# Kernel optimization log

Hardware: AMD Instinct MI355X
Metric: run time of the kernel (lower is better)

## Reference

```python
import jax, jax.numpy as jnp
import numpy as np

NUM_ORI = 16
DEGREE = 2
NUM_LAYERS = 2
LN_EPS = 1e-6


def ori_grid_s1(n):
    theta = jnp.linspace(0.0, 2.0 * jnp.pi, n + 1)[:-1]
    return jnp.stack([jnp.cos(theta), jnp.sin(theta)], axis=-1)  # (O, 2)


def poly_feats(z, degree):
    # PolynomialFeatures: [z, z*z outer, (z*z)*z outer ...] flattened
    feats = [z]
    p = z
    for _ in range(degree):
        p = (p[..., :, None] * z[..., None, :]).reshape(*z.shape[:-1], -1)
        feats.append(p)
    return jnp.concatenate(feats, axis=-1)


def basis_mlp(z, W1, b1, W2, b2):
    return jax.nn.gelu(jax.nn.gelu(z @ W1 + b1) @ W2 + b2)


def layer_norm(h, scale, bias):
    mu = h.mean(axis=-1, keepdims=True)
    var = ((h - mu) ** 2).mean(axis=-1, keepdims=True)
    return (h - mu) * jax.lax.rsqrt(var + LN_EPS) * scale + bias


def setup_inputs() -> dict:
    key = jax.random.key(0)
    ks = jax.random.split(key, 16)
    B, N, NIN, H, BD, WF, OUT, L = 1, 256, 3, 64, 32, 4, 3, NUM_LAYERS
    s = 0.05
    return {
        'pos': jax.random.normal(ks[0], (B, N, 2), jnp.float32),
        'x': jax.random.normal(ks[1], (B, N, NIN), jnp.float32),
        'skb_W1': jax.random.normal(ks[2], (14, H), jnp.float32) * s,
        'skb_b1': jnp.zeros((H,), jnp.float32),
        'skb_W2': jax.random.normal(ks[3], (H, BD), jnp.float32) * s,
        'skb_b2': jnp.zeros((BD,), jnp.float32),
        'rkb_W1': jax.random.normal(ks[4], (3, H), jnp.float32) * s,
        'rkb_b1': jnp.zeros((H,), jnp.float32),
        'rkb_W2': jax.random.normal(ks[5], (H, BD), jnp.float32) * s,
        'rkb_b2': jnp.zeros((BD,), jnp.float32),
        'emb_W': jax.random.normal(ks[6], (NIN, H), jnp.float32) * s,
        'conv_sW': jax.random.normal(ks[7], (L, BD, H), jnp.float32) * s,
        'conv_rW': jax.random.normal(ks[8], (L, BD, H), jnp.float32) * s,
        'conv_b': jnp.zeros((L, H), jnp.float32),
        'ln_scale': jnp.ones((L, H), jnp.float32),
        'ln_bias': jnp.zeros((L, H), jnp.float32),
        'lin1_W': jax.random.normal(ks[9], (L, H, WF * H), jnp.float32) * s,
        'lin1_b': jnp.zeros((L, WF * H), jnp.float32),
        'lin2_W': jax.random.normal(ks[10], (L, WF * H, H), jnp.float32) * s,
        'lin2_b': jnp.zeros((L, H), jnp.float32),
        'readout_W': jax.random.normal(ks[11], (H, OUT), jnp.float32) * s,
    }


def reference(pos, x, skb_W1, skb_b1, skb_W2, skb_b2, rkb_W1, rkb_b1, rkb_W2, rkb_b2,
              emb_W, conv_sW, conv_rW, conv_b, ln_scale, ln_bias,
              lin1_W, lin1_b, lin2_W, lin2_b, readout_W):
    ori = ori_grid_s1(NUM_ORI)  # (O, 2)
    # rel_pos: (B, n, m, 1, 2) -> broadcast against ori (O, 2)
    rel_pos = pos[:, None, :, None, :] - pos[:, :, None, None, :]
    inv1 = jnp.sum(rel_pos * ori[None, None, None, :, :], axis=-1, keepdims=True)  # (B,N,N,O,1)
    inv2 = jnp.linalg.norm(rel_pos - rel_pos * inv1, axis=-1, keepdims=True)       # (B,N,N,O,1)
    spatial_inv = jnp.concatenate([inv1, inv2], axis=-1)                            # (B,N,N,O,2)
    orient_inv = jnp.sum(ori[:, None, :] * ori[None, :, :], axis=-1, keepdims=True) # (O,O,1)

    kernel_basis = basis_mlp(poly_feats(spatial_inv, DEGREE), skb_W1, skb_b1, skb_W2, skb_b2)  # (B,N,N,O,BD)
    fiber_basis = basis_mlp(poly_feats(orient_inv, DEGREE), rkb_W1, rkb_b1, rkb_W2, rkb_b2)    # (O,O,BD)

    h = x @ emb_W                                  # (B,N,H)
    O = NUM_ORI
    h = jnp.broadcast_to(h[:, :, None, :], (h.shape[0], h.shape[1], O, h.shape[2]))  # (B,N,O,H)

    for i in range(NUM_LAYERS):
        inp = h
        sk = kernel_basis @ conv_sW[i]             # (B,N,N,O,H)
        rk = fiber_basis @ conv_rW[i]              # (O,O,H)
        c = jnp.einsum('bnoc,bmnoc->bmoc', h, sk)  # spatial aggregation
        c = jnp.einsum('bmoc,poc->bmpc', c, rk)    # orientation mixing
        c = c + conv_b[i]
        c = layer_norm(c, ln_scale[i], ln_bias[i])
        c = jax.nn.gelu(c @ lin1_W[i] + lin1_b[i]) @ lin2_W[i] + lin2_b[i]
        h = inp + c

    readout = h @ readout_W                        # (B,N,O,OUT)
    out_scalar = readout.mean(axis=-2)             # (B,N,OUT)
    out_scalar = jnp.sum(out_scalar, axis=1) / out_scalar.shape[1]  # global pool -> (B,OUT)
    return out_scalar
```

## Files before the change

### kernel.cpp

```cpp
#include <hip/hip_runtime.h>
#include <math.h>

#define NPTS 256
#define NORI 16
#define CH   64
#define BD   32
#define HID  64
#define STEP16 0.39269908169872414f

typedef __bf16 bf16x8 __attribute__((ext_vector_type(8)));
typedef float  f32x4  __attribute__((ext_vector_type(4)));

#define MFMA16(a, b, cc) __builtin_amdgcn_mfma_f32_16x16x32_bf16(a, b, cc, 0, 0, 0)
#define GLOAD_LDS16NT(g, l) \
    __builtin_amdgcn_global_load_lds((const __attribute__((address_space(1))) unsigned int*)(g), \
                                     (__attribute__((address_space(3))) unsigned int*)(l), 16, 0, 2)

__device__ __forceinline__ float gelu_f(float x) {
    float x2 = x * x;
    float y2 = x * fmaf(0.07135481627f, x2, 1.5957691216f);
    float e = __expf(y2);
    return x - x * __builtin_amdgcn_rcpf(e + 1.0f);
}

__device__ __forceinline__ unsigned pk2(float x, float y) {
    union { __bf16 h[2]; unsigned u; } r;
    r.h[0] = (__bf16)x; r.h[1] = (__bf16)y;
    return r.u;
}

__device__ __forceinline__ void dev_prep(
    const float* __restrict__ skb_W1, const float* __restrict__ skb_W2,
    const float* __restrict__ conv_sW,
    __bf16* __restrict__ w1T, __bf16* __restrict__ w2T, __bf16* __restrict__ w2Tlo,
    __bf16* __restrict__ sWT, __bf16* __restrict__ sWTlo, int t)
{
    if (t < 64) {
        float f[9];
        f[0] = skb_W1[t];
        f[1] = skb_W1[64 + t];
        f[2] = skb_W1[128 + t];
        f[3] = skb_W1[192 + t] + skb_W1[256 + t];
        f[4] = skb_W1[320 + t];
        f[5] = skb_W1[384 + t];
        f[6] = skb_W1[448 + t] + skb_W1[512 + t] + skb_W1[640 + t];
        f[7] = skb_W1[576 + t] + skb_W1[704 + t] + skb_W1[768 + t];
        f[8] = skb_W1[832 + t];
#pragma unroll
        for (int k = 0; k < 9; ++k) {
            __bf16 hi = (__bf16)f[k];
            w1T[t * 32 + k]      = hi;
            w1T[t * 32 + 9 + k]  = (__bf16)(f[k] - (float)hi);
            w1T[t * 32 + 18 + k] = hi;
        }
#pragma unroll
        for (int k = 27; k < 32; ++k) w1T[t * 32 + k] = (__bf16)0.0f;
    }
    for (int i = t; i < 2048; i += 256) {
        int n = i >> 6, kk = i & 63;
        float v = skb_W2[kk * 32 + n];
        __bf16 hi = (__bf16)v;
        w2T[i]   = hi;
        w2Tlo[i] = (__bf16)(v - (float)hi);
    }
    for (int i = t; i < 4096; i += 256) {
        int ll = i >> 11, chh = (i >> 5) & 63, k = i & 31;
        float v = conv_sW[(ll * 32 + k) * 64 + chh];
        __bf16 hi = (__bf16)v;
        sWT[i]   = hi;
        sWTlo[i] = (__bf16)(v - (float)hi);
    }
}

__device__ __forceinline__ void dev_fiber(
    const float* __restrict__ rkb_W1, const float* __restrict__ rkb_b1,
    const float* __restrict__ rkb_W2, const float* __restrict__ rkb_b2,
    const float* __restrict__ conv_rW, float* __restrict__ rk, int p, int t)
{
    __shared__ float w1L[3 * 64], b1L[64], w2L[64 * 32], b2L[32];
    __shared__ float rwL[2 * 32 * 64];
    __shared__ float t1L[16 * 64];
    __shared__ float fbL[16 * 32];

    if (t < 192) w1L[t] = rkb_W1[t];
    if (t >= 192 && t < 256) b1L[t - 192] = rkb_b1[t - 192];
    for (int i = t; i < 2048; i += 256) w2L[i] = rkb_W2[i];
    if (t < 32) b2L[t] = rkb_b2[t];
    for (int i = t; i < 4096; i += 256) rwL[i] = conv_rW[i];
    __syncthreads();

    const int o = t & 15;
    const float cp = cosf(p * STEP16), sp = sinf(p * STEP16);
    const float co = cosf(o * STEP16), so = sinf(o * STEP16);
    const float s0 = cp * co + sp * so;
    const float m1 = s0 * s0, m2 = m1 * s0;

    {
        const int jg = t >> 4;
#pragma unroll
        for (int u = 0; u < 4; ++u) {
            const int j = jg * 4 + u;
            float a = b1L[j] + s0 * w1L[j] + m1 * w1L[64 + j] + m2 * w1L[128 + j];
            t1L[o * 64 + j] = gelu_f(a);
        }
    }
    __syncthreads();
    {
        const int kg = t >> 4;
#pragma unroll
        for (int kk = 0; kk < 2; ++kk) {
            const int k = kg + kk * 16;
            float a = b2L[k];
#pragma unroll
            for (int j = 0; j < 64; ++j) a += t1L[o * 64 + j] * w2L[j * 32 + k];
            fbL[o * 32 + k] = gelu_f(a);
        }
    }
    __syncthreads();
    {
        const int o2 = t >> 4;
        const int chg = (t & 15) * 4;
#pragma unroll
        for (int l = 0; l < 2; ++l) {
            f32x4 acc = {0.f, 0.f, 0.f, 0.f};
#pragma unroll
            for (int k = 0; k < 32; ++k) {
                const float fv = fbL[o2 * 32 + k];
                const f32x4 rv = *(const f32x4*)(rwL + (l * 32 + k) * 64 + chg);
                acc[0] = fmaf(fv, rv[0], acc[0]);
                acc[1] = fmaf(fv, rv[1], acc[1]);
                acc[2] = fmaf(fv, rv[2], acc[2]);
                acc[3] = fmaf(fv, rv[3], acc[3]);
            }
            *(f32x4*)(rk + (l * 256 + p * 16 + o2) * 64 + chg) = acc;
        }
    }
}

__global__ __launch_bounds__(256) void k_prep(
    const float* __restrict__ skb_W1, const float* __restrict__ skb_W2,
    const float* __restrict__ conv_sW,
    __bf16* __restrict__ w1T, __bf16* __restrict__ w2T, __bf16* __restrict__ w2Tlo,
    __bf16* __restrict__ sWT, __bf16* __restrict__ sWTlo)
{
    dev_prep(skb_W1, skb_W2, conv_sW, w1T, w2T, w2Tlo, sWT, sWTlo, threadIdx.x);
}

__global__ __launch_bounds__(256) void k_fiber2(
    const float* __restrict__ rkb_W1, const float* __restrict__ rkb_b1,
    const float* __restrict__ rkb_W2, const float* __restrict__ rkb_b2,
    const float* __restrict__ conv_rW, float* __restrict__ rk)
{
    dev_fiber(rkb_W1, rkb_b1, rkb_W2, rkb_b2, conv_rW, rk, blockIdx.x, threadIdx.x);
}

__global__ __launch_bounds__(256) void k_init(
    const float* __restrict__ x, const float* __restrict__ emb_W, float* __restrict__ h)
{
    int idx = blockIdx.x * 256 + threadIdx.x;
    int ch = idx & 63;
    int n  = idx >> 10;
    h[idx] = x[n * 3] * emb_W[ch] + x[n * 3 + 1] * emb_W[64 + ch] + x[n * 3 + 2] * emb_W[128 + ch];
}

__global__ __launch_bounds__(256) void k_setup(
    const float* __restrict__ x, const float* __restrict__ emb_W, float* __restrict__ h2,
    const float* __restrict__ rkb_W1, const float* __restrict__ rkb_b1,
    const float* __restrict__ rkb_W2, const float* __restrict__ rkb_b2,
    const float* __restrict__ conv_rW, float* __restrict__ rk,
    const float* __restrict__ skb_W1, const float* __restrict__ skb_W2,
    const float* __restrict__ conv_sW,
    __bf16* __restrict__ w1T, __bf16* __restrict__ w2T, __bf16* __restrict__ w2Tlo,
    __bf16* __restrict__ sWT, __bf16* __restrict__ sWTlo)
{
    const int b = blockIdx.x, t = threadIdx.x;
    if (b < 1024) {
        int idx = b * 256 + t;
        int ch = (idx >> 4) & 63;
        int n  = idx >> 10;
        h2[idx] = x[n * 3] * emb_W[ch] + x[n * 3 + 1] * emb_W[64 + ch]
                + x[n * 3 + 2] * emb_W[128 + ch];
    } else if (b < 1040) {
        dev_fiber(rkb_W1, rkb_b1, rkb_W2, rkb_b2, conv_rW, rk, b - 1024, t);
    } else {
        dev_prep(skb_W1, skb_W2, conv_sW, w1T, w2T, w2Tlo, sWT, sWTlo, t);
    }
}

__global__ __launch_bounds__(256) void k_kb2(
    const float* __restrict__ pos,
    const float* __restrict__ skb_b1, const float* __restrict__ skb_b2,
    const __bf16* __restrict__ w1T, const __bf16* __restrict__ w2T,
    const __bf16* __restrict__ w2Tlo, __bf16* __restrict__ kb_g)
{
    const int t = threadIdx.x;
    const int c = t & 15, qq = (t >> 4) & 3, w = t >> 6;
    const int b = blockIdx.x;
    const int pair = b >> 2;
    const int ohalf = (b >> 1) & 1;
    const int mhalf = b & 1;
    const int m0 = (pair >> 4) * 16, n0 = (pair & 15) * 16;

    bf16x8 w1B[4], w2A[2][2], w2Alo[2][2];
    float b1x[4][4], b2x[2][4];
#pragma unroll
    for (int ni = 0; ni < 4; ++ni) {
        w1B[ni] = *(const bf16x8*)(w1T + (ni * 16 + c) * 32 + qq * 8);
#pragma unroll
        for (int r = 0; r < 4; ++r) b1x[ni][r] = skb_b1[ni * 16 + qq * 4 + r];
    }
#pragma unroll
    for (int mk = 0; mk < 2; ++mk) {
#pragma unroll
        for (int ks = 0; ks < 2; ++ks) {
            w2A[mk][ks]   = *(const bf16x8*)(w2T   + (mk * 16 + c) * 64 + ks * 32 + qq * 8);
            w2Alo[mk][ks] = *(const bf16x8*)(w2Tlo + (mk * 16 + c) * 64 + ks * 32 + qq * 8);
        }
#pragma unroll
        for (int r = 0; r < 4; ++r) b2x[mk][r] = skb_b2[mk * 16 + qq * 4 + r];
    }

    const int n = n0 + c;
    const float pnx = pos[2 * n], pny = pos[2 * n + 1];
    float cosv[4], sinv[4];
#pragma unroll
    for (int oi = 0; oi < 4; ++oi) {
        float th = (float)(ohalf * 4 + oi) * STEP16;
        cosv[oi] = cosf(th); sinv[oi] = sinf(th);
    }
    const int s0lane = c + ((qq & 1) << 5);
    const int s1lane = s0lane + 16;
    const int selhi = qq >> 1;
    const f32x4 zf = {0.f, 0.f, 0.f, 0.f};

#pragma unroll 1
    for (int mi2 = 0; mi2 < 2; ++mi2) {
        const int m = m0 + w * 4 + mhalf * 2 + mi2;
        const float dx = pnx - pos[2 * m];
        const float dy = pny - pos[2 * m + 1];
#pragma unroll
        for (int oi = 0; oi < 4; ++oi) {
            const int o = ohalf * 4 + oi;
            float a = dx * cosv[oi] + dy * sinv[oi];
            float vx = dx - dx * a, vy = dy - dy * a;
            float b2 = sqrtf(vx * vx + vy * vy);
            float mfv[9];
            mfv[0] = a; mfv[1] = b2; mfv[2] = a * a; mfv[3] = a * b2; mfv[4] = b2 * b2;
            mfv[5] = mfv[2] * a; mfv[6] = mfv[2] * b2; mfv[7] = mfv[3] * b2; mfv[8] = mfv[4] * b2;
            __bf16 mh[9], ml[9];
#pragma unroll
            for (int i = 0; i < 9; ++i) {
                mh[i] = (__bf16)mfv[i];
                ml[i] = (__bf16)(mfv[i] - (float)mh[i]);
            }
            bf16x8 mb;
            if (qq == 0) {
                mb[0]=mh[0]; mb[1]=mh[1]; mb[2]=mh[2]; mb[3]=mh[3];
                mb[4]=mh[4]; mb[5]=mh[5]; mb[6]=mh[6]; mb[7]=mh[7];
            } else if (qq == 1) {
                mb[0]=mh[8]; mb[1]=mh[0]; mb[2]=mh[1]; mb[3]=mh[2];
                mb[4]=mh[3]; mb[5]=mh[4]; mb[6]=mh[5]; mb[7]=mh[6];
            } else if (qq == 2) {
                mb[0]=mh[7]; mb[1]=mh[8]; mb[2]=ml[0]; mb[3]=ml[1];
                mb[4]=ml[2]; mb[5]=ml[3]; mb[6]=ml[4]; mb[7]=ml[5];
            } else {
                mb[0]=ml[6]; mb[1]=ml[7]; mb[2]=ml[8]; mb[3]=(__bf16)0.0f;
                mb[4]=(__bf16)0.0f; mb[5]=(__bf16)0.0f; mb[6]=(__bf16)0.0f; mb[7]=(__bf16)0.0f;
            }

            unsigned t1p[4][2];
#pragma unroll
            for (int ni = 0; ni < 4; ++ni) {
                f32x4 acc = MFMA16(w1B[ni], mb, zf);
                float g0 = gelu_f(acc[0] + b1x[ni][0]);
                float g1 = gelu_f(acc[1] + b1x[ni][1]);
                float g2 = gelu_f(acc[2] + b1x[ni][2]);
                float g3 = gelu_f(acc[3] + b1x[ni][3]);
                t1p[ni][0] = pk2(g0, g1);
                t1p[ni][1] = pk2(g2, g3);
            }

            bf16x8 B2[2];
#pragma unroll
            for (int ks = 0; ks < 2; ++ks) {
                const unsigned lo0 = t1p[ks * 2][0],     lo1 = t1p[ks * 2][1];
                const unsigned hi0 = t1p[ks * 2 + 1][0], hi1 = t1p[ks * 2 + 1][1];
                unsigned aL0 = (unsigned)__shfl((int)lo0, s0lane);
                unsigned aL1 = (unsigned)__shfl((int)lo1, s0lane);
                unsigned aL2 = (unsigned)__shfl((int)lo0, s1lane);
                unsigned aL3 = (unsigned)__shfl((int)lo1, s1lane);
                unsigned aH0 = (unsigned)__shfl((int)hi0, s0lane);
                unsigned aH1 = (unsigned)__shfl((int)hi1, s0lane);
                unsigned aH2 = (unsigned)__shfl((int)hi0, s1lane);
                unsigned aH3 = (unsigned)__shfl((int)hi1, s1lane);
                union { unsigned u[4]; bf16x8 v; } bu;
                bu.u[0] = selhi ? aH0 : aL0;
                bu.u[1] = selhi ? aH1 : aL1;
                bu.u[2] = selhi ? aH2 : aL2;
                bu.u[3] = selhi ? aH3 : aL3;
                B2[ks] = bu.v;
            }

            const size_t ptP = (size_t)((m * 256 + n) * 16 + o);
            const size_t ptM = (size_t)((n * 256 + m) * 16 + (o ^ 8));
            const int swz = o & 3;
#pragma unroll
            for (int mk = 0; mk < 2; ++mk) {
                f32x4 acc = MFMA16(w2A[mk][0], B2[0], zf);
                acc = MFMA16(w2A[mk][1], B2[1], acc);
                acc = MFMA16(w2Alo[mk][0], B2[0], acc);
                acc = MFMA16(w2Alo[mk][1], B2[1], acc);
                float g0 = gelu_f(acc[0] + b2x[mk][0]);
                float g1 = gelu_f(acc[1] + b2x[mk][1]);
                float g2 = gelu_f(acc[2] + b2x[mk][2]);
                float g3 = gelu_f(acc[3] + b2x[mk][3]);
                uint2 pv; pv.x = pk2(g0, g1); pv.y = pk2(g2, g3);
                const int off = (((mk * 2 + (qq >> 1)) ^ swz) << 4) + ((qq & 1) << 3);
                *(uint2*)((char*)kb_g + ptP * 64 + off) = pv;
                *(uint2*)((char*)kb_g + ptM * 64 + off) = pv;
            }
        }
    }
}

__global__ __launch_bounds__(1024) void k_conv4(
    const __bf16* __restrict__ kb_g,
    const __bf16* __restrict__ sWT, const __bf16* __restrict__ sWTlo,
    const float* __restrict__ conv_b, const float* __restrict__ rkg,
    const float* __restrict__ ln_scale, const float* __restrict__ ln_bias,
    const float* __restrict__ lin1_W, const float* __restrict__ lin1_b,
    const float* __restrict__ lin2_W, const float* __restrict__ lin2_b,
    const float* __restrict__ h_in, float* __restrict__ h_out, int l)
{
    __shared__ __align__(16) unsigned char smem[90112];
    const int t = threadIdx.x;
    const int m = blockIdx.x;
    const int w = t >> 6, lane = t & 63;
    const int qq = lane >> 4, c = lane & 15;
    const f32x4 zf = {0.f, 0.f, 0.f, 0.f};

    bf16x8 sWB[4], sWBlo[4];
#pragma unroll
    for (int ni = 0; ni < 4; ++ni) {
        sWB[ni]   = *(const bf16x8*)(sWT   + l * 2048 + (ni * 16 + c) * 32 + qq * 8);
        sWBlo[ni] = *(const bf16x8*)(sWTlo + l * 2048 + (ni * 16 + c) * 32 + qq * 8);
    }

    f32x4 cacc[4];
#pragma unroll
    for (int ni = 0; ni < 4; ++ni)
#pragma unroll
        for (int r = 0; r < 4; ++r) cacc[ni][r] = 0.f;

    const char* kbm = (const char*)kb_g + (size_t)m * 262144;
    const char* gsrc0 = kbm + w * 1024 + lane * 16;
    char* lbase = (char*)smem + w * 1024;
    const int myrow = (w * 16 + c) * 64 + ((qq ^ (c & 3)) << 4);

    GLOAD_LDS16NT(gsrc0, lbase);
    f32x4 hc0, hc1, hc2, hc3;
    {
        const float* hp = h_in + w * 1024 + c * 16 + qq * 4;
        hc0 = *(const f32x4*)(hp);
        hc1 = *(const f32x4*)(hp + 256);
        hc2 = *(const f32x4*)(hp + 512);
        hc3 = *(const f32x4*)(hp + 768);
    }

#pragma unroll 1
    for (int tile = 0; tile < 15; ++tile) {
        const int bufoff = (tile & 1) << 14;
        GLOAD_LDS16NT(gsrc0 + (size_t)(tile + 1) * 16384, lbase + (bufoff ^ 16384));
        asm volatile("s_waitcnt vmcnt(5)" ::: "memory");
        __builtin_amdgcn_sched_barrier(0);
        bf16x8 aF = *(const bf16x8*)(smem + bufoff + myrow);

        const float* hpn = h_in + ((tile + 1) * 16 + w) * 1024 + c * 16 + qq * 4;
        f32x4 hn0 = *(const f32x4*)(hpn);
        f32x4 hn1 = *(const f32x4*)(hpn + 256);
        f32x4 hn2 = *(const f32x4*)(hpn + 512);
        f32x4 hn3 = *(const f32x4*)(hpn + 768);

        f32x4 g;
        g = MFMA16(aF, sWB[0], zf);
        g = MFMA16(aF, sWBlo[0], g);
#pragma unroll
        for (int r = 0; r < 4; ++r) cacc[0][r] = fmaf(g[r], hc0[r], cacc[0][r]);
        g = MFMA16(aF, sWB[1], zf);
        g = MFMA16(aF, sWBlo[1], g);
#pragma unroll
        for (int r = 0; r < 4; ++r) cacc[1][r] = fmaf(g[r], hc1[r], cacc[1][r]);
        g = MFMA16(aF, sWB[2], zf);
        g = MFMA16(aF, sWBlo[2], g);
#pragma unroll
        for (int r = 0; r < 4; ++r) cacc[2][r] = fmaf(g[r], hc2[r], cacc[2][r]);
        g = MFMA16(aF, sWB[3], zf);
        g = MFMA16(aF, sWBlo[3], g);
#pragma unroll
        for (int r = 0; r < 4; ++r) cacc[3][r] = fmaf(g[r], hc3[r], cacc[3][r]);

        hc0 = hn0; hc1 = hn1; hc2 = hn2; hc3 = hn3;
    }
    {
        asm volatile("s_waitcnt vmcnt(4)" ::: "memory");
        __builtin_amdgcn_sched_barrier(0);
        bf16x8 aF = *(const bf16x8*)(smem + ((15 & 1) << 14) + myrow);
        f32x4 g;
        g = MFMA16(aF, sWB[0], zf);
        g = MFMA16(aF, sWBlo[0], g);
#pragma unroll
        for (int r = 0; r < 4; ++r) cacc[0][r] = fmaf(g[r], hc0[r], cacc[0][r]);
        g = MFMA16(aF, sWB[1], zf);
        g = MFMA16(aF, sWBlo[1], g);
#pragma unroll
        for (int r = 0; r < 4; ++r) cacc[1][r] = fmaf(g[r], hc1[r], cacc[1][r]);
        g = MFMA16(aF, sWB[2], zf);
        g = MFMA16(aF, sWBlo[2], g);
#pragma unroll
        for (int r = 0; r < 4; ++r) cacc[2][r] = fmaf(g[r], hc2[r], cacc[2][r]);
        g = MFMA16(aF, sWB[3], zf);
        g = MFMA16(aF, sWBlo[3], g);
#pragma unroll
        for (int r = 0; r < 4; ++r) cacc[3][r] = fmaf(g[r], hc3[r], cacc[3][r]);
    }
    __syncthreads();

    {
        float* c1p = (float*)smem;
#pragma unroll
        for (int ni = 0; ni < 4; ++ni)
#pragma unroll
            for (int r = 0; r < 4; ++r)
                c1p[w * 1024 + (qq * 4 + r) * 64 + ni * 16 + c] = cacc[ni][r];
    }
    __syncthreads();
    {
        float* c1p = (float*)smem;
        float* c1r = (float*)(smem + 65536);
        float s = 0.f;
#pragma unroll
        for (int ww = 0; ww < 16; ++ww) s += c1p[ww * 1024 + t];
        c1r[t] = s;
    }
    __syncthreads();

    {
        float* c1r = (float*)(smem + 65536);
        float* cns = (float*)(smem + 69632);
        const int ch = lane;
        const float cb  = conv_b[l * 64 + ch];
        const float lsc = ln_scale[l * 64 + ch], lbi = ln_bias[l * 64 + ch];
        const float* rkp = rkg + (l * 256 + w * 16) * 64 + ch;
        float s = cb;
#pragma unroll
        for (int o = 0; o < 16; ++o) s += c1r[o * 64 + ch] * rkp[o * 64];
        float red = s;
#pragma unroll
        for (int off = 32; off > 0; off >>= 1) red += __shfl_xor(red, off);
        float mu = red * (1.0f / 64.0f);
        float d = s - mu;
        float r2 = d * d;
#pragma unroll
        for (int off = 32; off > 0; off >>= 1) r2 += __shfl_xor(r2, off);
        cns[w * 64 + ch] = d * rsqrtf(r2 * (1.0f / 64.0f) + 1e-6f) * lsc + lbi;
    }
    __syncthreads();

    {
        float* cns = (float*)(smem + 69632);
        float* usS = (float*)(smem + 73728);
        const int j = t & 255, q4 = t >> 8;
        const float* W1l = lin1_W + l * 64 * 256;
        const float bl1 = lin1_b[l * 256 + j];
        float ua[4];
#pragma unroll
        for (int pi = 0; pi < 4; ++pi) ua[pi] = bl1;
#pragma unroll 4
        for (int c2 = 0; c2 < 64; ++c2) {
            const float wv = W1l[c2 * 256 + j];
#pragma unroll
            for (int pi = 0; pi < 4; ++pi)
                ua[pi] = fmaf(cns[(q4 * 4 + pi) * 64 + c2], wv, ua[pi]);
        }
#pragma unroll
        for (int pi = 0; pi < 4; ++pi) usS[(q4 * 4 + pi) * 256 + j] = gelu_f(ua[pi]);
    }
    __syncthreads();

    {
        float* usS = (float*)(smem + 73728);
        const int ch2 = t & 63, pg = t >> 6;
        const float* W2l = lin2_W + l * 256 * 64;
        float o0 = lin2_b[l * 64 + ch2];
#pragma unroll 4
        for (int j = 0; j < 256; ++j)
            o0 = fmaf(usS[pg * 256 + j], W2l[j * 64 + ch2], o0);
        const int i0 = m * 1024 + ch2 * 16 + pg;
        h_out[i0] = h_in[i0] + o0;
    }
}

__global__ __launch_bounds__(512, 1) void k_layer2(
    const float* __restrict__ pos,
    const float* __restrict__ skb_b1, const float* __restrict__ skb_b2,
    const __bf16* __restrict__ w1T, const __bf16* __restrict__ w2T,
    const __bf16* __restrict__ w2Tlo,
    const __bf16* __restrict__ sWT, const __bf16* __restrict__ sWTlo,
    const float* __restrict__ conv_b, const float* __restrict__ rkg,
    const float* __restrict__ ln_scale, const float* __restrict__ ln_bias,
    const float* __restrict__ lin1_W, const float* __restrict__ lin1_b,
    const float* __restrict__ lin2_W, const float* __restrict__ lin2_b,
    const float* __restrict__ h_in, float* __restrict__ h_out, int l)
{
    __shared__ __align__(16) unsigned char smem[57344];
    const int t = threadIdx.x;
    const int m = blockIdx.x;
    const int w = t >> 6, lane = t & 63;
    const int qq = lane >> 4, c = lane & 15;

    bf16x8 w1B[4], sWB[4], sWBlo[4], w2B[2][2], w2Blo[2][2];
    float b1v[4], b2v[2];
#pragma unroll
    for (int ni = 0; ni < 4; ++ni) {
        w1B[ni]   = *(const bf16x8*)(w1T + (ni * 16 + c) * 32 + qq * 8);
        sWB[ni]   = *(const bf16x8*)(sWT   + l * 2048 + (ni * 16 + c) * 32 + qq * 8);
        sWBlo[ni] = *(const bf16x8*)(sWTlo + l * 2048 + (ni * 16 + c) * 32 + qq * 8);
        b1v[ni] = skb_b1[ni * 16 + c];
    }
#pragma unroll
    for (int nt = 0; nt < 2; ++nt) {
        b2v[nt] = skb_b2[nt * 16 + c];
#pragma unroll
        for (int ks = 0; ks < 2; ++ks) {
            w2B[nt][ks]   = *(const bf16x8*)(w2T   + (nt * 16 + c) * 64 + ks * 32 + qq * 8);
            w2Blo[nt][ks] = *(const bf16x8*)(w2Tlo + (nt * 16 + c) * 64 + ks * 32 + qq * 8);
        }
    }

    const float pmx = pos[2 * m], pmy = pos[2 * m + 1];
    float co_ = 0.f, so_ = 0.f;
    if (t < 256) { float th = (float)(t & 15) * STEP16; co_ = cosf(th); so_ = sinf(th); }

    f32x4 cacc[4];
#pragma unroll
    for (int ni = 0; ni < 4; ++ni)
#pragma unroll
        for (int r = 0; r < 4; ++r) cacc[ni][r] = 0.f;

#pragma unroll 1
    for (int tile = 0; tile < 16; ++tile) {
        if (t < 256) {
            const int n = tile * 16 + (t >> 4);
            float dx = pos[2 * n] - pmx, dy = pos[2 * n + 1] - pmy;
            float a = dx * co_ + dy * so_;
            float vx = dx - dx * a, vy = dy - dy * a;
            float b = sqrtf(vx * vx + vy * vy);
            float mf[9];
            mf[0] = a; mf[1] = b; mf[2] = a * a; mf[3] = a * b; mf[4] = b * b;
            mf[5] = mf[2] * a; mf[6] = mf[2] * b; mf[7] = mf[3] * b; mf[8] = mf[4] * b;
            __bf16 s[32];
#pragma unroll
            for (int i = 0; i < 9; ++i) {
                __bf16 hi = (__bf16)mf[i];
                s[i] = hi; s[9 + i] = hi;
                s[18 + i] = (__bf16)(mf[i] - (float)hi);
            }
#pragma unroll
            for (int i = 27; i < 32; ++i) s[i] = (__bf16)0.0f;
            unsigned char* rowp = smem + t * 64;
#pragma unroll
            for (int u = 0; u < 4; ++u) {
                bf16x8 vv;
#pragma unroll
                for (int j = 0; j < 8; ++j) vv[j] = s[u * 8 + j];
                *(bf16x8*)(rowp + ((u ^ (t & 3)) << 4)) = vv;
            }
        }
        __syncthreads();

#pragma unroll
        for (int mm = 0; mm < 2; ++mm) {
            const int row = (2 * w + mm) * 16 + c;
            bf16x8 aF = *(const bf16x8*)(smem + row * 64 + ((qq ^ (row & 3)) << 4));
#pragma unroll
            for (int ni = 0; ni < 4; ++ni) {
                f32x4 acc = {0.f, 0.f, 0.f, 0.f};
                acc = MFMA16(aF, w1B[ni], acc);
#pragma unroll
                for (int r = 0; r < 4; ++r) {
                    const int ro = (2 * w + mm) * 16 + qq * 4 + r;
                    float g = gelu_f(acc[r] + b1v[ni]);
                    const int chc = ni * 16 + c;
                    *(__bf16*)(smem + 16384 + ro * 128 + (((chc >> 3) ^ (ro & 7)) << 4)
                               + ((chc & 7) << 1)) = (__bf16)g;
                }
            }
        }
        __syncthreads();

#pragma unroll
        for (int mm = 0; mm < 2; ++mm) {
            const int row = (2 * w + mm) * 16 + c;
            bf16x8 a0 = *(const bf16x8*)(smem + 16384 + row * 128 + ((qq ^ (row & 7)) << 4));
            bf16x8 a1 = *(const bf16x8*)(smem + 16384 + row * 128 + (((4 + qq) ^ (row & 7)) << 4));
#pragma unroll
            for (int nt = 0; nt < 2; ++nt) {
                f32x4 acc = {0.f, 0.f, 0.f, 0.f};
                acc = MFMA16(a0, w2B[nt][0], acc);
                acc = MFMA16(a1, w2B[nt][1], acc);
                acc = MFMA16(a0, w2Blo[nt][0], acc);
                acc = MFMA16(a1, w2Blo[nt][1], acc);
#pragma unroll
                for (int r = 0; r < 4; ++r) {
                    const int ro = (2 * w + mm) * 16 + qq * 4 + r;
                    float g = gelu_f(acc[r] + b2v[nt]);
                    const int kc = nt * 16 + c;
                    *(__bf16*)(smem + ro * 64 + (((kc >> 3) ^ (ro & 3)) << 4)
                               + ((kc & 7) << 1)) = (__bf16)g;
                }
            }
        }
        __syncthreads();

#pragma unroll
        for (int mm = 0; mm < 2; ++mm) {
            const int mi = 2 * w + mm;
            const int row = mi * 16 + c;
            bf16x8 aF = *(const bf16x8*)(smem + row * 64 + ((qq ^ (row & 3)) << 4));
            const int nbase = (tile * 16 + mi) * 1024 + qq * 256;
#pragma unroll
            for (int ni = 0; ni < 4; ++ni) {
                f32x4 g3 = {0.f, 0.f, 0.f, 0.f};
                g3 = MFMA16(aF, sWB[ni], g3);
                g3 = MFMA16(aF, sWBlo[ni], g3);
#pragma unroll
                for (int r = 0; r < 4; ++r) {
                    float hv = h_in[nbase + r * 64 + ni * 16 + c];
                    cacc[ni][r] = fmaf(g3[r], hv, cacc[ni][r]);
                }
            }
        }
        __syncthreads();
    }

    {
        float* c1p = (float*)smem;
#pragma unroll
        for (int ni = 0; ni < 4; ++ni)
#pragma unroll
            for (int r = 0; r < 4; ++r)
                c1p[w * 1024 + (qq * 4 + r) * 64 + ni * 16 + c] = cacc[ni][r];
    }
    __syncthreads();
    {
        float* c1p = (float*)smem;
        float* c1r = (float*)(smem + 32768);
        for (int i = t; i < 1024; i += 512) {
            float s = 0.f;
#pragma unroll
            for (int ww = 0; ww < 8; ++ww) s += c1p[ww * 1024 + i];
            c1r[i] = s;
        }
    }
    __syncthreads();

    {
        float* c1r = (float*)(smem + 32768);
        float* cns = (float*)(smem + 36864);
        const int ch = lane;
        const float cb  = conv_b[l * 64 + ch];
        const float lsc = ln_scale[l * 64 + ch], lbi = ln_bias[l * 64 + ch];
#pragma unroll
        for (int pp = 0; pp < 2; ++pp) {
            const int p = w + pp * 8;
            const float* rkp = rkg + (l * 256 + p * 16) * 64 + ch;
            float s = cb;
#pragma unroll
            for (int o = 0; o < 16; ++o) s += c1r[o * 64 + ch] * rkp[o * 64];
            float red = s;
#pragma unroll
            for (int off = 32; off > 0; off >>= 1) red += __shfl_xor(red, off);
            float mu = red * (1.0f / 64.0f);
            float d = s - mu;
            float r2 = d * d;
#pragma unroll
            for (int off = 32; off > 0; off >>= 1) r2 += __shfl_xor(r2, off);
            cns[p * 64 + ch] = d * rsqrtf(r2 * (1.0f / 64.0f) + 1e-6f) * lsc + lbi;
        }
    }
    __syncthreads();

    {
        float* cns = (float*)(smem + 36864);
        float* usS = (float*)(smem + 40960);
        const int j = t & 255, half = t >> 8;
        const float* W1l = lin1_W + l * 64 * 256;
        const float bl1 = lin1_b[l * 256 + j];
        float ua[8];
#pragma unroll
        for (int pi = 0; pi < 8; ++pi) ua[pi] = bl1;
#pragma unroll 1
        for (int c2 = 0; c2 < 64; ++c2) {
            const float wv = W1l[c2 * 256 + j];
#pragma unroll
            for (int pi = 0; pi < 8; ++pi)
                ua[pi] = fmaf(cns[(half * 8 + pi) * 64 + c2], wv, ua[pi]);
        }
#pragma unroll
        for (int pi = 0; pi < 8; ++pi) usS[(half * 8 + pi) * 256 + j] = gelu_f(ua[pi]);
    }
    __syncthreads();

    {
        float* usS = (float*)(smem + 40960);
        const int ch2 = t & 63, pg = t >> 6;
        const float* W2l = lin2_W + l * 256 * 64;
        const float bl2 = lin2_b[l * 64 + ch2];
        float o0 = bl2, o1 = bl2;
#pragma unroll 2
        for (int j = 0; j < 256; ++j) {
            const float wv = W2l[j * 64 + ch2];
            o0 = fmaf(usS[pg * 256 + j], wv, o0);
            o1 = fmaf(usS[(pg + 8) * 256 + j], wv, o1);
        }
        const int i0 = (m * 16 + pg) * 64 + ch2;
        const int i1 = (m * 16 + pg + 8) * 64 + ch2;
        h_out[i0] = h_in[i0] + o0;
        h_out[i1] = h_in[i1] + o1;
    }
}

__global__ __launch_bounds__(256) void k_readout_part(
    const float* __restrict__ h, float* __restrict__ part16)
{
    __shared__ float part[4][64];
    const int t = threadIdx.x, b = blockIdx.x;
    const int c = t & 63, seg = t >> 6;
    float s = 0.f;
    const int r0 = b * 256 + seg * 64;
    for (int r = r0; r < r0 + 64; ++r) s += h[r * 64 + c];
    part[seg][c] = s;
    __syncthreads();
    if (t < 64) part16[b * 64 + t] = part[0][t] + part[1][t] + part[2][t] + part[3][t];
}

__global__ __launch_bounds__(256) void k_readout_part2(
    const float* __restrict__ h, float* __restrict__ part16)
{
    const int t = threadIdx.x, b = blockIdx.x;
    const int ch = t >> 2, oq = t & 3;
    float s = 0.f;
#pragma unroll
    for (int nn = 0; nn < 16; ++nn) {
        const int n = b * 16 + nn;
        f32x4 v = *(const f32x4*)(h + n * 1024 + ch * 16 + oq * 4);
        s += (v[0] + v[1]) + (v[2] + v[3]);
    }
    s += __shfl_xor(s, 1);
    s += __shfl_xor(s, 2);
    if (oq == 0) part16[b * 64 + ch] = s;
}

__global__ __launch_bounds__(64) void k_readout_final(
    const float* __restrict__ part16, const float* __restrict__ rW, float* __restrict__ out)
{
    __shared__ float hbar[64];
    const int t = threadIdx.x;
    float s = 0.f;
#pragma unroll
    for (int b = 0; b < 16; ++b) s += part16[b * 64 + t];
    hbar[t] = s * (1.0f / 4096.0f);
    __syncthreads();
    if (t < 3) {
        float s2 = 0.f;
#pragma unroll
        for (int k = 0; k < 64; ++k) s2 += hbar[k] * rW[k * 3 + t];
        out[t] = s2;
    }
}

extern "C" void kernel_launch(void* const* d_in, const int* in_sizes, int n_in,
                              void* d_out, int out_size, void* d_ws, size_t ws_size,
                              hipStream_t stream)
{
    const float* pos      = (const float*)d_in[0];
    const float* x        = (const float*)d_in[1];
    const float* skb_W1   = (const float*)d_in[2];
    const float* skb_b1   = (const float*)d_in[3];
    const float* skb_W2   = (const float*)d_in[4];
    const float* skb_b2   = (const float*)d_in[5];
    const float* rkb_W1   = (const float*)d_in[6];
    const float* rkb_b1   = (const float*)d_in[7];
    const float* rkb_W2   = (const float*)d_in[8];
    const float* rkb_b2   = (const float*)d_in[9];
    const float* emb_W    = (const float*)d_in[10];
    const float* conv_sW  = (const float*)d_in[11];
    const float* conv_rW  = (const float*)d_in[12];
    const float* conv_b   = (const float*)d_in[13];
    const float* ln_scale = (const float*)d_in[14];
    const float* ln_bias  = (const float*)d_in[15];
    const float* lin1_W   = (const float*)d_in[16];
    const float* lin1_b   = (const float*)d_in[17];
    const float* lin2_W   = (const float*)d_in[18];
    const float* lin2_b   = (const float*)d_in[19];
    const float* readout_W= (const float*)d_in[20];
    float* out = (float*)d_out;

    unsigned char* ws = (unsigned char*)d_ws;
    float*  h_a    = (float*)(ws);
    float*  h_b    = (float*)(ws + 1048576);
    float*  rkw    = (float*)(ws + 2097152);
    __bf16* w1T    = (__bf16*)(ws + 2228224);
    __bf16* w2T    = (__bf16*)(ws + 2232320);
    __bf16* w2Tlo  = (__bf16*)(ws + 2236416);
    __bf16* sWT    = (__bf16*)(ws + 2240512);
    __bf16* sWTlo  = (__bf16*)(ws + 2248704);
    float*  part16 = (float*)(ws + 2256896);
    __bf16* kb_g   = (__bf16*)(ws + 2260992);

    const bool fast = (ws_size >= 2260992ull + 67108864ull);

    if (fast) {
        k_setup<<<1041, 256, 0, stream>>>(x, emb_W, h_a,
                                          rkb_W1, rkb_b1, rkb_W2, rkb_b2, conv_rW, rkw,
                                          skb_W1, skb_W2, conv_sW,
                                          w1T, w2T, w2Tlo, sWT, sWTlo);
        k_kb2<<<1024, 256, 0, stream>>>(pos, skb_b1, skb_b2, w1T, w2T, w2Tlo, kb_g);
        k_conv4<<<256, 1024, 0, stream>>>(kb_g, sWT, sWTlo, conv_b, rkw,
                                          ln_scale, ln_bias, lin1_W, lin1_b,
                                          lin2_W, lin2_b, h_a, h_b, 0);
        k_conv4<<<256, 1024, 0, stream>>>(kb_g, sWT, sWTlo, conv_b, rkw,
                                          ln_scale, ln_bias, lin1_W, lin1_b,
                                          lin2_W, lin2_b, h_b, h_a, 1);
        k_readout_part2<<<16, 256, 0, stream>>>(h_a, part16);
        k_readout_final<<<1, 64, 0, stream>>>(part16, readout_W, out);
    } else {
        k_prep<<<1, 256, 0, stream>>>(skb_W1, skb_W2, conv_sW, w1T, w2T, w2Tlo, sWT, sWTlo);
        k_fiber2<<<16, 256, 0, stream>>>(rkb_W1, rkb_b1, rkb_W2, rkb_b2, conv_rW, rkw);
        k_init<<<1024, 256, 0, stream>>>(x, emb_W, h_a);
        k_layer2<<<256, 512, 0, stream>>>(pos, skb_b1, skb_b2, w1T, w2T, w2Tlo, sWT, sWTlo,
                                          conv_b, rkw, ln_scale, ln_bias, lin1_W, lin1_b,
                                          lin2_W, lin2_b, h_a, h_b, 0);
        k_layer2<<<256, 512, 0, stream>>>(pos, skb_b1, skb_b2, w1T, w2T, w2Tlo, sWT, sWTlo,
                                          conv_b, rkw, ln_scale, ln_bias, lin1_W, lin1_b,
                                          lin2_W, lin2_b, h_b, h_a, 1);
        k_readout_part<<<16, 256, 0, stream>>>(h_a, part16);
        k_readout_final<<<1, 64, 0, stream>>>(part16, readout_W, out);
    }
}
```

Before: 146.2 us.

## Split conv kernel into half-N aggregation blocks plus separate epilogue kernel

The fused per-point conv kernel is split in two. The spatial aggregation now runs over 512 blocks, each covering half of the neighbour range and writing partial sums to a global workspace. A separate epilogue kernel adds the two halves and does orientation mixing, layer norm and the MLP. The aim is more parallelism and occupancy (launch bounds allow 2 blocks per CU, with smaller LDS) and overlap of the memory-bound kb streaming. The cost is two extra kernel launches per forward pass and a global round-trip of the partial sums.

Result: slower. 162.5 us (+11.2%).

```diff
diff --git a/kernel.cpp b/kernel.cpp
--- a/kernel.cpp
+++ b/kernel.cpp
@@ -323,180 +323,199 @@
     }
 }
 
-__global__ __launch_bounds__(1024) void k_conv4(
+__global__ __launch_bounds__(1024, 2) void k_convm(
     const __bf16* __restrict__ kb_g,
     const __bf16* __restrict__ sWT, const __bf16* __restrict__ sWTlo,
+    const float* __restrict__ h_in, float* __restrict__ c1part, int l)
+{
+    __shared__ __align__(16) unsigned char smem[65536];
+    const int t = threadIdx.x;
+    const int m = blockIdx.x >> 1, half = blockIdx.x & 1;
+    const int w = t >> 6, lane = t & 63;
+    const int qq = lane >> 4, c = lane & 15;
+    const f32x4 zf = {0.f, 0.f, 0.f, 0.f};
+
+    bf16x8 sWB[4], sWBlo[4];
+#pragma unroll
+    for (int ni = 0; ni < 4; ++ni) {
+        sWB[ni]   = *(const bf16x8*)(sWT   + l * 2048 + (ni * 16 + c) * 32 + qq * 8);
+        sWBlo[ni] = *(const bf16x8*)(sWTlo + l * 2048 + (ni * 16 + c) * 32 + qq * 8);
+    }
+
+    f32x4 cacc[4];
+#pragma unroll
+    for (int ni = 0; ni < 4; ++ni)
+#pragma unroll
+        for (int r = 0; r < 4; ++r) cacc[ni][r] = 0.f;
+
+    const char* kbm = (const char*)kb_g + (size_t)m * 262144 + (size_t)half * 131072;
+    const char* gsrc0 = kbm + w * 1024 + lane * 16;
+    char* lbase = (char*)smem + w * 1024;
+    const int myrow = (w * 16 + c) * 64 + ((qq ^ (c & 3)) << 4);
+    const int n00 = half * 128 + w;
+
+    GLOAD_LDS16NT(gsrc0, lbase);
+    f32x4 hc0, hc1, hc2, hc3;
+    {
+        const float* hp = h_in + n00 * 1024 + c * 16 + qq * 4;
+        hc0 = *(const f32x4*)(hp);
+        hc1 = *(const f32x4*)(hp + 256);
+        hc2 = *(const f32x4*)(hp + 512);
+        hc3 = *(const f32x4*)(hp + 768);
+    }
+
+#pragma unroll 1
+    for (int tt = 0; tt < 7; ++tt) {
+        const int bufoff = (tt & 1) << 14;
+        GLOAD_LDS16NT(gsrc0 + (size_t)(tt + 1) * 16384, lbase + (bufoff ^ 16384));
+        asm volatile("s_waitcnt vmcnt(5)" ::: "memory");
+        __builtin_amdgcn_sched_barrier(0);
+        bf16x8 aF = *(const bf16x8*)(smem + bufoff + myrow);
+
+        const float* hpn = h_in + (n00 + (tt + 1) * 16) * 1024 + c * 16 + qq * 4;
+        f32x4 hn0 = *(const f32x4*)(hpn);
+        f32x4 hn1 = *(const f32x4*)(hpn + 256);
+        f32x4 hn2 = *(const f32x4*)(hpn + 512);
+        f32x4 hn3 = *(const f32x4*)(hpn + 768);
+
+        f32x4 g;
+        g = MFMA16(aF, sWB[0], zf);
+        g = MFMA16(aF, sWBlo[0], g);
+#pragma unroll
+        for (int r = 0; r < 4; ++r) cacc[0][r] = fmaf(g[r], hc0[r], cacc[0][r]);
+        g = MFMA16(aF, sWB[1], zf);
+        g = MFMA16(aF, sWBlo[1], g);
+#pragma unroll
+        for (int r = 0; r < 4; ++r) cacc[1][r] = fmaf(g[r], hc1[r], cacc[1][r]);
+        g = MFMA16(aF, sWB[2], zf);
+        g = MFMA16(aF, sWBlo[2], g);
+#pragma unroll
+        for (int r = 0; r < 4; ++r) cacc[2][r] = fmaf(g[r], hc2[r], cacc[2][r]);
+        g = MFMA16(aF, sWB[3], zf);
+        g = MFMA16(aF, sWBlo[3], g);
+#pragma unroll
+        for (int r = 0; r < 4; ++r) cacc[3][r] = fmaf(g[r], hc3[r], cacc[3][r]);
+
+        hc0 = hn0; hc1 = hn1; hc2 = hn2; hc3 = hn3;
+    }
+    {
+        asm volatile("s_waitcnt vmcnt(4)" ::: "memory");
+        __builtin_amdgcn_sched_barrier(0);
+        bf16x8 aF = *(const bf16x8*)(smem + ((7 & 1) << 14) + myrow);
+        f32x4 g;
+        g = MFMA16(aF, sWB[0], zf);
+        g = MFMA16(aF, sWBlo[0], g);
+#pragma unroll
+        for (int r = 0; r < 4; ++r) cacc[0][r] = fmaf(g[r], hc0[r], cacc[0][r]);
+        g = MFMA16(aF, sWB[1], zf);
+        g = MFMA16(aF, sWBlo[1], g);
+#pragma unroll
+        for (int r = 0; r < 4; ++r) cacc[1][r] = fmaf(g[r], hc1[r], cacc[1][r]);
+        g = MFMA16(aF, sWB[2], zf);
+        g = MFMA16(aF, sWBlo[2], g);
+#pragma unroll
+        for (int r = 0; r < 4; ++r) cacc[2][r] = fmaf(g[r], hc2[r], cacc[2][r]);
+        g = MFMA16(aF, sWB[3], zf);
+        g = MFMA16(aF, sWBlo[3], g);
+#pragma unroll
+        for (int r = 0; r < 4; ++r) cacc[3][r] = fmaf(g[r], hc3[r], cacc[3][r]);
+    }
+    __syncthreads();
+
+    {
+        float* c1p = (float*)smem;
+#pragma unroll
+        for (int ni = 0; ni < 4; ++ni)
+#pragma unroll
+            for (int r = 0; r < 4; ++r)
+                c1p[w * 1024 + (qq * 4 + r) * 64 + ni * 16 + c] = cacc[ni][r];
+    }
+    __syncthreads();
+    {
+        float* c1p = (float*)smem;
+        float s = 0.f;
+#pragma unroll
+        for (int ww = 0; ww < 16; ++ww) s += c1p[ww * 1024 + t];
+        c1part[(half * 256 + m) * 1024 + t] = s;
+    }
+}
+
+__global__ __launch_bounds__(512) void k_convepi(
+    const float* __restrict__ c1part,
     const float* __restrict__ conv_b, const float* __restrict__ rkg,
     const float* __restrict__ ln_scale, const float* __restrict__ ln_bias,
     const float* __restrict__ lin1_W, const float* __restrict__ lin1_b,
     const float* __restrict__ lin2_W, const float* __restrict__ lin2_b,
     const float* __restrict__ h_in, float* __restrict__ h_out, int l)
 {
-    __shared__ __align__(16) unsigned char smem[90112];
+    __shared__ float c1r[1024];
+    __shared__ float cns[1024];
+    __shared__ float usS[4096];
     const int t = threadIdx.x;
     const int m = blockIdx.x;
     const int w = t >> 6, lane = t & 63;
-    const int qq = lane >> 4, c = lane & 15;
-    const f32x4 zf = {0.f, 0.f, 0.f, 0.f};
-
-    bf16x8 sWB[4], sWBlo[4];
-#pragma unroll
-    for (int ni = 0; ni < 4; ++ni) {
-        sWB[ni]   = *(const bf16x8*)(sWT   + l * 2048 + (ni * 16 + c) * 32 + qq * 8);
-        sWBlo[ni] = *(const bf16x8*)(sWTlo + l * 2048 + (ni * 16 + c) * 32 + qq * 8);
-    }
-
-    f32x4 cacc[4];
-#pragma unroll
-    for (int ni = 0; ni < 4; ++ni)
-#pragma unroll
-        for (int r = 0; r < 4; ++r) cacc[ni][r] = 0.f;
-
-    const char* kbm = (const char*)kb_g + (size_t)m * 262144;
-    const char* gsrc0 = kbm + w * 1024 + lane * 16;
-    char* lbase = (char*)smem + w * 1024;
-    const int myrow = (w * 16 + c) * 64 + ((qq ^ (c & 3)) << 4);
-
-    GLOAD_LDS16NT(gsrc0, lbase);
-    f32x4 hc0, hc1, hc2, hc3;
-    {
-        const float* hp = h_in + w * 1024 + c * 16 + qq * 4;
-        hc0 = *(const f32x4*)(hp);
-        hc1 = *(const f32x4*)(hp + 256);
-        hc2 = *(const f32x4*)(hp + 512);
-        hc3 = *(const f32x4*)(hp + 768);
-    }
-
-#pragma unroll 1
-    for (int tile = 0; tile < 15; ++tile) {
-        const int bufoff = (tile & 1) << 14;
-        GLOAD_LDS16NT(gsrc0 + (size_t)(tile + 1) * 16384, lbase + (bufoff ^ 16384));
-        asm volatile("s_waitcnt vmcnt(5)" ::: "memory");
-        __builtin_amdgcn_sched_barrier(0);
-        bf16x8 aF = *(const bf16x8*)(smem + bufoff + myrow);
-
-        const float* hpn = h_in + ((tile + 1) * 16 + w) * 1024 + c * 16 + qq * 4;
-        f32x4 hn0 = *(const f32x4*)(hpn);
-        f32x4 hn1 = *(const f32x4*)(hpn + 256);
-        f32x4 hn2 = *(const f32x4*)(hpn + 512);
-        f32x4 hn3 = *(const f32x4*)(hpn + 768);
-
-        f32x4 g;
-        g = MFMA16(aF, sWB[0], zf);
-        g = MFMA16(aF, sWBlo[0], g);
-#pragma unroll
-        for (int r = 0; r < 4; ++r) cacc[0][r] = fmaf(g[r], hc0[r], cacc[0][r]);
-        g = MFMA16(aF, sWB[1], zf);
-        g = MFMA16(aF, sWBlo[1], g);
-#pragma unroll
-        for (int r = 0; r < 4; ++r) cacc[1][r] = fmaf(g[r], hc1[r], cacc[1][r]);
-        g = MFMA16(aF, sWB[2], zf);
-        g = MFMA16(aF, sWBlo[2], g);
-#pragma unroll
-        for (int r = 0; r < 4; ++r) cacc[2][r] = fmaf(g[r], hc2[r], cacc[2][r]);
-        g = MFMA16(aF, sWB[3], zf);
-        g = MFMA16(aF, sWBlo[3], g);
-#pragma unroll
-        for (int r = 0; r < 4; ++r) cacc[3][r] = fmaf(g[r], hc3[r], cacc[3][r]);
-
-        hc0 = hn0; hc1 = hn1; hc2 = hn2; hc3 = hn3;
-    }
-    {
-        asm volatile("s_waitcnt vmcnt(4)" ::: "memory");
-        __builtin_amdgcn_sched_barrier(0);
-        bf16x8 aF = *(const bf16x8*)(smem + ((15 & 1) << 14) + myrow);
-        f32x4 g;
-        g = MFMA16(aF, sWB[0], zf);
-        g = MFMA16(aF, sWBlo[0], g);
-#pragma unroll
-        for (int r = 0; r < 4; ++r) cacc[0][r] = fmaf(g[r], hc0[r], cacc[0][r]);
-        g = MFMA16(aF, sWB[1], zf);
-        g = MFMA16(aF, sWBlo[1], g);
-#pragma unroll
-        for (int r = 0; r < 4; ++r) cacc[1][r] = fmaf(g[r], hc1[r], cacc[1][r]);
-        g = MFMA16(aF, sWB[2], zf);
-        g = MFMA16(aF, sWBlo[2], g);
-#pragma unroll
-        for (int r = 0; r < 4; ++r) cacc[2][r] = fmaf(g[r], hc2[r], cacc[2][r]);
-        g = MFMA16(aF, sWB[3], zf);
-        g = MFMA16(aF, sWBlo[3], g);
-#pragma unroll
-        for (int r = 0; r < 4; ++r) cacc[3][r] = fmaf(g[r], hc3[r], cacc[3][r]);
-    }
-    __syncthreads();
-
-    {
-        float* c1p = (float*)smem;
-#pragma unroll
-        for (int ni = 0; ni < 4; ++ni)
-#pragma unroll
-            for (int r = 0; r < 4; ++r)
-                c1p[w * 1024 + (qq * 4 + r) * 64 + ni * 16 + c] = cacc[ni][r];
-    }
-    __syncthreads();
-    {
-        float* c1p = (float*)smem;
-        float* c1r = (float*)(smem + 65536);
-        float s = 0.f;
-#pragma unroll
-        for (int ww = 0; ww < 16; ++ww) s += c1p[ww * 1024 + t];
-        c1r[t] = s;
-    }
-    __syncthreads();
-
-    {
-        float* c1r = (float*)(smem + 65536);
-        float* cns = (float*)(smem + 69632);
+
+    for (int i = t; i < 1024; i += 512)
+        c1r[i] = c1part[m * 1024 + i] + c1part[(256 + m) * 1024 + i];
+    __syncthreads();
+
+    {
         const int ch = lane;
         const float cb  = conv_b[l * 64 + ch];
         const float lsc = ln_scale[l * 64 + ch], lbi = ln_bias[l * 64 + ch];
-        const float* rkp = rkg + (l * 256 + w * 16) * 64 + ch;
-        float s = cb;
-#pragma unroll
-        for (int o = 0; o < 16; ++o) s += c1r[o * 64 + ch] * rkp[o * 64];
-        float red = s;
-#pragma unroll
-        for (int off = 32; off > 0; off >>= 1) red += __shfl_xor(red, off);
-        float mu = red * (1.0f / 64.0f);
-        float d = s - mu;
-        float r2 = d * d;
-#pragma unroll
-        for (int off = 32; off > 0; off >>= 1) r2 += __shfl_xor(r2, off);
-        cns[w * 64 + ch] = d * rsqrtf(r2 * (1.0f / 64.0f) + 1e-6f) * lsc + lbi;
-    }
-    __syncthreads();
-
-    {
-        float* cns = (float*)(smem + 69632);
-        float* usS = (float*)(smem + 73728);
-        const int j = t & 255, q4 = t >> 8;
+#pragma unroll
+        for (int pp = 0; pp < 2; ++pp) {
+            const int p = w + pp * 8;
+            const float* rkp = rkg + (l * 256 + p * 16) * 64 + ch;
+            float s = cb;
+#pragma unroll
+            for (int o = 0; o < 16; ++o) s += c1r[o * 64 + ch] * rkp[o * 64];
+            float red = s;
+#pragma unroll
+            for (int off = 32; off > 0; off >>= 1) red += __shfl_xor(red, off);
+            float mu = red * (1.0f / 64.0f);
+            float d = s - mu;
+            float r2 = d * d;
+#pragma unroll
+            for (int off = 32; off > 0; off >>= 1) r2 += __shfl_xor(r2, off);
+            cns[p * 64 + ch] = d * rsqrtf(r2 * (1.0f / 64.0f) + 1e-6f) * lsc + lbi;
+        }
+    }
+    __syncthreads();
+
+    {
+        const int j = t & 255, hf = t >> 8;
         const float* W1l = lin1_W + l * 64 * 256;
         const float bl1 = lin1_b[l * 256 + j];
-        float ua[4];
-#pragma unroll
-        for (int pi = 0; pi < 4; ++pi) ua[pi] = bl1;
+        float ua[8];
+#pragma unroll
+        for (int pi = 0; pi < 8; ++pi) ua[pi] = bl1;
 #pragma unroll 4
         for (int c2 = 0; c2 < 64; ++c2) {
             const float wv = W1l[c2 * 256 + j];
 #pragma unroll
-            for (int pi = 0; pi < 4; ++pi)
-                ua[pi] = fmaf(cns[(q4 * 4 + pi) * 64 + c2], wv, ua[pi]);
-        }
-#pragma unroll
-        for (int pi = 0; pi < 4; ++pi) usS[(q4 * 4 + pi) * 256 + j] = gelu_f(ua[pi]);
-    }
-    __syncthreads();
-
-    {
-        float* usS = (float*)(smem + 73728);
+            for (int pi = 0; pi < 8; ++pi)
+                ua[pi] = fmaf(cns[(hf * 8 + pi) * 64 + c2], wv, ua[pi]);
+        }
+#pragma unroll
+        for (int pi = 0; pi < 8; ++pi) usS[(hf * 8 + pi) * 256 + j] = gelu_f(ua[pi]);
+    }
+    __syncthreads();
+
+    {
         const int ch2 = t & 63, pg = t >> 6;
         const float* W2l = lin2_W + l * 256 * 64;
-        float o0 = lin2_b[l * 64 + ch2];
+        const float bl2 = lin2_b[l * 64 + ch2];
+        float o0 = bl2, o1 = bl2;
 #pragma unroll 4
-        for (int j = 0; j < 256; ++j)
-            o0 = fmaf(usS[pg * 256 + j], W2l[j * 64 + ch2], o0);
+        for (int j = 0; j < 256; ++j) {
+            const float wv = W2l[j * 64 + ch2];
+            o0 = fmaf(usS[pg * 256 + j], wv, o0);
+            o1 = fmaf(usS[(pg + 8) * 256 + j], wv, o1);
+        }
         const int i0 = m * 1024 + ch2 * 16 + pg;
-        h_out[i0] = h_in[i0] + o0;
+        h_out[i0]     = h_in[i0]     + o0;
+        h_out[i0 + 8] = h_in[i0 + 8] + o1;
     }
 }
 
@@ -817,8 +836,9 @@
     __bf16* sWTlo  = (__bf16*)(ws + 2248704);
     float*  part16 = (float*)(ws + 2256896);
     __bf16* kb_g   = (__bf16*)(ws + 2260992);
-
-    const bool fast = (ws_size >= 2260992ull + 67108864ull);
+    float*  c1part = (float*)(ws + 69369856);
+
+    const bool fast = (ws_size >= 71467008ull);
 
     if (fast) {
         k_setup<<<1041, 256, 0, stream>>>(x, emb_W, h_a,
@@ -826,12 +846,12 @@
                                           skb_W1, skb_W2, conv_sW,
                                           w1T, w2T, w2Tlo, sWT, sWTlo);
         k_kb2<<<1024, 256, 0, stream>>>(pos, skb_b1, skb_b2, w1T, w2T, w2Tlo, kb_g);
-        k_conv4<<<256, 1024, 0, stream>>>(kb_g, sWT, sWTlo, conv_b, rkw,
-                                          ln_scale, ln_bias, lin1_W, lin1_b,
-                                          lin2_W, lin2_b, h_a, h_b, 0);
-        k_conv4<<<256, 1024, 0, stream>>>(kb_g, sWT, sWTlo, conv_b, rkw,
-                                          ln_scale, ln_bias, lin1_W, lin1_b,
-                                          lin2_W, lin2_b, h_b, h_a, 1);
+        k_convm<<<512, 1024, 0, stream>>>(kb_g, sWT, sWTlo, h_a, c1part, 0);
+        k_convepi<<<256, 512, 0, stream>>>(c1part, conv_b, rkw, ln_scale, ln_bias,
+                                           lin1_W, lin1_b, lin2_W, lin2_b, h_a, h_b, 0);
+        k_convm<<<512, 1024, 0, stream>>>(kb_g, sWT, sWTlo, h_b, c1part, 1);
+        k_convepi<<<256, 512, 0, stream>>>(c1part, conv_b, rkw, ln_scale, ln_bias,
+                                           lin1_W, lin1_b, lin2_W, lin2_b, h_b, h_a, 1);
         k_readout_part2<<<16, 256, 0, stream>>>(h_a, part16);
         k_readout_final<<<1, 64, 0, stream>>>(part16, readout_W, out);
     } else {
```
